# Performance work log

Measured on AMD Instinct MI355X. Metric: run time of the kernel, lower is better.

Reference implementation:

```python
import jax, jax.numpy as jnp
import numpy as np

BS, N_AGENTS, SA_DIM, HID = 2048, 64, 128, 256


def setup_inputs() -> dict:
    key = jax.random.key(0)
    ks = jax.random.split(key, 16)
    s = lambda fan_in: 1.0 / np.sqrt(fan_in)
    u = lambda k, shp, b: jax.random.uniform(k, shp, jnp.float32, -b, b)
    return {
        "x": jax.random.normal(ks[0], (BS, N_AGENTS, SA_DIM), jnp.float32),
        # encoder: Linear(sa, hid) -> Linear(hid, hid)
        "enc_w1": u(ks[1], (SA_DIM, HID), s(SA_DIM)),
        "enc_b1": u(ks[2], (HID,), s(SA_DIM)),
        "enc_w2": u(ks[3], (HID, HID), s(HID)),
        "enc_b2": u(ks[4], (HID,), s(HID)),
        # attention 'general' linear_in (no bias)
        "attn_w": u(ks[5], (HID, HID), s(HID)),
        # gc1: Linear(sa, hid); nn_gc1: Linear(sa, hid)
        "gc1_w": u(ks[6], (SA_DIM, HID), s(SA_DIM)),
        "gc1_b": u(ks[7], (HID,), s(SA_DIM)),
        "nn1_w": u(ks[8], (SA_DIM, HID), s(SA_DIM)),
        "nn1_b": u(ks[9], (HID,), s(SA_DIM)),
        # gc2: Linear(hid, hid); nn_gc2: Linear(hid, hid)
        "gc2_w": u(ks[10], (HID, HID), s(HID)),
        "gc2_b": u(ks[11], (HID,), s(HID)),
        "nn2_w": u(ks[12], (HID, HID), s(HID)),
        "nn2_b": u(ks[13], (HID,), s(HID)),
        "n_agents": N_AGENTS,
    }


def reference(x, enc_w1, enc_b1, enc_w2, enc_b2, attn_w,
              gc1_w, gc1_b, nn1_w, nn1_b, gc2_w, gc2_b, nn2_w, nn2_b,
              n_agents):
    relu = jax.nn.relu
    inv_n = 1.0 / n_agents
    # encoder MLP: relu(relu(x W1 + b1) W2 + b2)  -> [bs, n, hid]
    emb = relu(relu(x @ enc_w1 + enc_b1) @ enc_w2 + enc_b2)
    # general attention: softmax((emb W_a) emb^T) over last axis -> [bs, n, n]
    scores = jnp.einsum('bnd,bmd->bnm', emb @ attn_w, emb)
    attn = jax.nn.softmax(scores, axis=-1)
    # gc1: adj @ Linear(x); residual relu branch; normalize by n_agents
    feat = relu(jnp.einsum('bnm,bmh->bnh', attn, x @ gc1_w + gc1_b))
    feat = (feat + relu(x @ nn1_w + nn1_b)) * inv_n
    # gc2 on feat
    out = relu(jnp.einsum('bnm,bmh->bnh', attn, feat @ gc2_w + gc2_b))
    out = (out + relu(feat @ nn2_w + nn2_b)) * inv_n
    return out, attn
```

## Files before the change

kernel.cpp:

```cpp
#include <hip/hip_runtime.h>

typedef _Float16 half8 __attribute__((ext_vector_type(8)));
typedef _Float16 half4_t __attribute__((ext_vector_type(4)));
typedef float f32x4 __attribute__((ext_vector_type(4)));

#define NBATCH 2048
#define NA 64
#define SA 128
#define HID 256

#define OFF_X 0
#define OFF_R0 8192
#define OFF_ATT (8192 + 16384)
#define SMEM_BYTES ((8192 + 16384 + 8192) * 2)

#define W_ENC1 0
#define W_ENC2 (W_ENC1 + 128 * 256)
#define W_ATTN (W_ENC2 + 256 * 256)
#define W_GC1 (W_ATTN + 256 * 256)
#define W_NN1 (W_GC1 + 128 * 256)
#define W_GC2 (W_NN1 + 128 * 256)
#define W_NN2 (W_GC2 + 256 * 256)

#define MFMA(a, b, cacc) __builtin_amdgcn_mfma_f32_16x16x32_f16((a), (b), (cacc), 0, 0, 0)

__global__ void pack_all(const float* __restrict__ e1, const float* __restrict__ e2,
                         const float* __restrict__ aw, const float* __restrict__ g1,
                         const float* __restrict__ n1, const float* __restrict__ g2,
                         const float* __restrict__ n2, _Float16* __restrict__ dst) {
  int b = (int)blockIdx.x;
  const float* src;
  int off;
  if (b < 16) { src = e1; off = W_ENC1; }
  else if (b < 48) { src = e2; off = W_ENC2; b -= 16; }
  else if (b < 80) { src = aw; off = W_ATTN; b -= 48; }
  else if (b < 96) { src = g1; off = W_GC1; b -= 80; }
  else if (b < 112) { src = n1; off = W_NN1; b -= 96; }
  else if (b < 144) { src = g2; off = W_GC2; b -= 112; }
  else { src = n2; off = W_NN2; b -= 144; }
  int t = b * 256 + (int)threadIdx.x;
  int lane = t & 63, frag = t >> 6;
  int nt = frag & 15, kt = frag >> 4;
  int g = lane >> 4, c = lane & 15;
  half8 h;
#pragma unroll
  for (int j = 0; j < 8; ++j)
    h[j] = (_Float16)src[(size_t)(kt * 32 + g * 8 + j) * 256 + nt * 16 + c];
  *(half8*)(dst + off + (size_t)t * 8) = h;
}

__global__ __launch_bounds__(256, 2) void dicg_main(
    const float* __restrict__ x, const float* __restrict__ b_enc1,
    const float* __restrict__ b_enc2, const float* __restrict__ b_gc1,
    const float* __restrict__ b_nn1, const float* __restrict__ b_gc2,
    const float* __restrict__ b_nn2, const _Float16* __restrict__ wp,
    float* __restrict__ out, float* __restrict__ attn_out) {
  extern __shared__ _Float16 sm[];
  _Float16* X = sm + OFF_X;
  _Float16* R0 = sm + OFF_R0;
  _Float16* ATTp = sm + OFF_ATT;

  const int tid = (int)threadIdx.x;
  const int wv = tid >> 6;
  const int lane = tid & 63;
  const int g = lane >> 4;
  const int c = lane & 15;
  const int bb = (int)blockIdx.x;
  const float* __restrict__ xb = x + (size_t)bb * (NA * SA);

  auto ldA = [&](const _Float16* p, int kt, int rt) -> half8 {
    return *(const half8*)(p + (kt * 4 + rt) * 512 + lane * 8);
  };
  auto ldB = [&](const _Float16* p, int kt, int ct) -> half8 {
    return *(const half8*)(p + (kt * 16 + ct) * 512 + lane * 8);
  };
  auto wfrag = [&](const _Float16* wb, int kt, int ntg) -> half8 {
    return *(const half8*)(wb + ((size_t)(kt * 16 + ntg) * 64 + lane) * 8);
  };
  auto xfrag = [&](int r0, int k0) -> half8 {
    const float* p = xb + (r0 + c) * SA + k0 + g * 8;
    f32x4 u = *(const f32x4*)p;
    f32x4 v = *(const f32x4*)(p + 4);
    half8 h;
    h[0] = (_Float16)u[0]; h[1] = (_Float16)u[1];
    h[2] = (_Float16)u[2]; h[3] = (_Float16)u[3];
    h[4] = (_Float16)v[0]; h[5] = (_Float16)v[1];
    h[6] = (_Float16)v[2]; h[7] = (_Float16)v[3];
    return h;
  };

  auto stA_val = [&](_Float16* dst, int rt, int nt, int r, float v) {
    int kt = 2 * wv + (nt >> 1);
    int lanep = (2 * (nt & 1) + (c >> 3)) * 16 + 4 * g + r;
    dst[(kt * 4 + rt) * 512 + lanep * 8 + (c & 7)] = (_Float16)v;
  };
  auto ep_storeA = [&](f32x4(&acc)[4][4], const float* bias, bool dorelu) {
#pragma unroll
    for (int nt = 0; nt < 4; ++nt) {
      float bv = bias[64 * wv + 16 * nt + c];
#pragma unroll
      for (int rt = 0; rt < 4; ++rt)
#pragma unroll
        for (int r = 0; r < 4; ++r) {
          float y = acc[rt][nt][r] + bv;
          if (dorelu) y = fmaxf(y, 0.f);
          stA_val(R0, rt, nt, r, y);
        }
    }
  };
  auto ep_storeB = [&](f32x4(&acc)[4][4], const float* bias) {
#pragma unroll
    for (int nt = 0; nt < 4; ++nt) {
      float bv = bias[64 * wv + 16 * nt + c];
#pragma unroll
      for (int rt = 0; rt < 4; ++rt) {
        half4_t h;
#pragma unroll
        for (int r = 0; r < 4; ++r) h[r] = (_Float16)(acc[rt][nt][r] + bv);
        int fi = (rt >> 1) * 16 + 4 * wv + nt;
        int lanep = (2 * (rt & 1) + (g >> 1)) * 16 + c;
        *(half4_t*)(R0 + fi * 512 + lanep * 8 + 4 * (g & 1)) = h;
      }
    }
  };
  auto stQ = [&](const f32x4(&q2)[2], int s) {
    _Float16* base = ATTp + (8 + 2 * wv + s) * 512;
#pragma unroll
    for (int nt2 = 0; nt2 < 2; ++nt2)
#pragma unroll
      for (int r = 0; r < 4; ++r)
        base[((2 * nt2 + (c >> 3)) * 16 + 4 * g + r) * 8 + (c & 7)] = (_Float16)q2[nt2][r];
  };

  auto mmA = [&](f32x4(&acc)[4][4], const _Float16* Ap, const _Float16* wb, int nkt) {
#pragma unroll
    for (int kt = 0; kt < nkt; ++kt) {
      half8 af[4], bf[4];
#pragma unroll
      for (int rt = 0; rt < 4; ++rt) af[rt] = ldA(Ap, kt, rt);
#pragma unroll
      for (int nt = 0; nt < 4; ++nt) bf[nt] = wfrag(wb, kt, 4 * wv + nt);
#pragma unroll
      for (int rt = 0; rt < 4; ++rt)
#pragma unroll
        for (int nt = 0; nt < 4; ++nt) acc[rt][nt] = MFMA(af[rt], bf[nt], acc[rt][nt]);
    }
  };
  auto mmA2 = [&](f32x4(&a1)[4][4], f32x4(&a2)[4][4], const _Float16* Ap,
                  const _Float16* wb1, const _Float16* wb2, int nkt) {
#pragma unroll
    for (int kt = 0; kt < nkt; ++kt) {
      half8 af[4], b1[4], b2[4];
#pragma unroll
      for (int rt = 0; rt < 4; ++rt) af[rt] = ldA(Ap, kt, rt);
#pragma unroll
      for (int nt = 0; nt < 4; ++nt) b1[nt] = wfrag(wb1, kt, 4 * wv + nt);
#pragma unroll
      for (int nt = 0; nt < 4; ++nt) b2[nt] = wfrag(wb2, kt, 4 * wv + nt);
#pragma unroll
      for (int rt = 0; rt < 4; ++rt)
#pragma unroll
        for (int nt = 0; nt < 4; ++nt) {
          a1[rt][nt] = MFMA(af[rt], b1[nt], a1[rt][nt]);
          a2[rt][nt] = MFMA(af[rt], b2[nt], a2[rt][nt]);
        }
    }
  };
  auto mm_att = [&](f32x4(&acc)[4][4]) {
#pragma unroll
    for (int kt = 0; kt < 2; ++kt) {
      half8 af[4], bf[4];
#pragma unroll
      for (int rt = 0; rt < 4; ++rt) af[rt] = ldA(ATTp, kt, rt);
#pragma unroll
      for (int nt = 0; nt < 4; ++nt) bf[nt] = ldB(R0, kt, 4 * wv + nt);
#pragma unroll
      for (int rt = 0; rt < 4; ++rt)
#pragma unroll
        for (int nt = 0; nt < 4; ++nt) acc[rt][nt] = MFMA(af[rt], bf[nt], acc[rt][nt]);
    }
  };

  {
    f32x4 acc[4][4]{};
#pragma unroll
    for (int kt = 0; kt < 4; ++kt) {
      half8 af[4], bf[4];
#pragma unroll
      for (int rt = 0; rt < 4; ++rt) af[rt] = xfrag(16 * rt, kt * 32);
#pragma unroll
      for (int nt = 0; nt < 4; ++nt) bf[nt] = wfrag(wp + W_ENC1, kt, 4 * wv + nt);
      if (kt == wv) {
#pragma unroll
        for (int rt = 0; rt < 4; ++rt)
          *(half8*)(X + (kt * 4 + rt) * 512 + lane * 8) = af[rt];
      }
#pragma unroll
      for (int rt = 0; rt < 4; ++rt)
#pragma unroll
        for (int nt = 0; nt < 4; ++nt) acc[rt][nt] = MFMA(af[rt], bf[nt], acc[rt][nt]);
    }
    ep_storeA(acc, b_enc1, true);
  }
  __syncthreads();
  {
    f32x4 acc[4][4]{};
    mmA(acc, R0, wp + W_ENC2, 8);
    __syncthreads();
    ep_storeA(acc, b_enc2, true);
  }
  __syncthreads();
  {
    half8 aeK[8];
#pragma unroll
    for (int k2 = 0; k2 < 8; ++k2) aeK[k2] = ldA(R0, k2, wv);
    f32x4 sc[4]{};
    {
      f32x4 q2[2]{};
#pragma unroll
      for (int k2 = 0; k2 < 8; ++k2) {
        q2[0] = MFMA(aeK[k2], wfrag(wp + W_ATTN, k2, 0), q2[0]);
        q2[1] = MFMA(aeK[k2], wfrag(wp + W_ATTN, k2, 1), q2[1]);
      }
      stQ(q2, 0);
    }
#pragma unroll
    for (int ktp = 0; ktp < 8; ++ktp) {
      f32x4 q2n[2]{};
      if (ktp < 7) {
#pragma unroll
        for (int k2 = 0; k2 < 8; ++k2) {
          q2n[0] = MFMA(aeK[k2], wfrag(wp + W_ATTN, k2, 2 * ktp + 2), q2n[0]);
          q2n[1] = MFMA(aeK[k2], wfrag(wp + W_ATTN, k2, 2 * ktp + 3), q2n[1]);
        }
      }
      asm volatile("s_waitcnt lgkmcnt(0)" ::: "memory");
      half8 qb = *(const half8*)(ATTp + (8 + 2 * wv + (ktp & 1)) * 512 + lane * 8);
      if (ktp < 7) stQ(q2n, (ktp + 1) & 1);
#pragma unroll
      for (int rt = 0; rt < 4; ++rt) sc[rt] = MFMA(ldA(R0, ktp, rt), qb, sc[rt]);
    }
    float m = sc[0][0];
#pragma unroll
    for (int rt = 0; rt < 4; ++rt)
#pragma unroll
      for (int r = 0; r < 4; ++r) m = fmaxf(m, sc[rt][r]);
    m = fmaxf(m, __shfl_xor(m, 16));
    m = fmaxf(m, __shfl_xor(m, 32));
    float e[4][4], s = 0.f;
#pragma unroll
    for (int rt = 0; rt < 4; ++rt)
#pragma unroll
      for (int r = 0; r < 4; ++r) {
        e[rt][r] = __expf(sc[rt][r] - m);
        s += e[rt][r];
      }
    s += __shfl_xor(s, 16);
    s += __shfl_xor(s, 32);
    float inv = 1.0f / s;
    float* ao = attn_out + ((size_t)bb * NA + 16 * wv + c) * NA;
#pragma unroll
    for (int rt = 0; rt < 4; ++rt) {
      f32x4 vv;
      half4_t hh;
#pragma unroll
      for (int r = 0; r < 4; ++r) {
        vv[r] = e[rt][r] * inv;
        hh[r] = (_Float16)vv[r];
      }
      *(f32x4*)(ao + 16 * rt + 4 * g) = vv;
      int fi = (rt >> 1) * 4 + wv;
      int lanep = (2 * (rt & 1) + (g >> 1)) * 16 + c;
      *(half4_t*)(ATTp + fi * 512 + lanep * 8 + 4 * (g & 1)) = hh;
    }
  }
  __syncthreads();
  {
    f32x4 aG[4][4]{}, aN[4][4]{};
    mmA2(aG, aN, X, wp + W_GC1, wp + W_NN1, 4);
    ep_storeB(aG, b_gc1);
    half4_t r2h[4][4];
#pragma unroll
    for (int nt = 0; nt < 4; ++nt) {
      float bv = b_nn1[64 * wv + 16 * nt + c];
#pragma unroll
      for (int rt = 0; rt < 4; ++rt)
#pragma unroll
        for (int r = 0; r < 4; ++r)
          r2h[rt][nt][r] = (_Float16)fmaxf(aN[rt][nt][r] + bv, 0.f);
    }
    __syncthreads();
    f32x4 a1[4][4]{};
    mm_att(a1);
    __syncthreads();
#pragma unroll
    for (int nt = 0; nt < 4; ++nt)
#pragma unroll
      for (int rt = 0; rt < 4; ++rt)
#pragma unroll
        for (int r = 0; r < 4; ++r)
          stA_val(R0, rt, nt, r,
                  (fmaxf(a1[rt][nt][r], 0.f) + (float)r2h[rt][nt][r]) * 0.015625f);
  }
  __syncthreads();
  {
    f32x4 aN[4][4]{}, aG[4][4]{};
    mmA2(aN, aG, R0, wp + W_NN2, wp + W_GC2, 8);
    half4_t r2h[4][4];
#pragma unroll
    for (int nt = 0; nt < 4; ++nt) {
      float bv = b_nn2[64 * wv + 16 * nt + c];
#pragma unroll
      for (int rt = 0; rt < 4; ++rt)
#pragma unroll
        for (int r = 0; r < 4; ++r)
          r2h[rt][nt][r] = (_Float16)fmaxf(aN[rt][nt][r] + bv, 0.f);
    }
    __syncthreads();
    ep_storeB(aG, b_gc2);
    __syncthreads();
    f32x4 a1[4][4]{};
    mm_att(a1);
    float* ob = out + (size_t)bb * NA * HID;
#pragma unroll
    for (int nt = 0; nt < 4; ++nt)
#pragma unroll
      for (int rt = 0; rt < 4; ++rt)
#pragma unroll
        for (int r = 0; r < 4; ++r)
          ob[(size_t)(16 * rt + 4 * g + r) * HID + 64 * wv + 16 * nt + c] =
              (fmaxf(a1[rt][nt][r], 0.f) + (float)r2h[rt][nt][r]) * 0.015625f;
  }
}

extern "C" void kernel_launch(void* const* d_in, const int* in_sizes, int n_in,
                              void* d_out, int out_size, void* d_ws, size_t ws_size,
                              hipStream_t stream) {
  const float* x = (const float*)d_in[0];
  const float* enc_w1 = (const float*)d_in[1];
  const float* enc_b1 = (const float*)d_in[2];
  const float* enc_w2 = (const float*)d_in[3];
  const float* enc_b2 = (const float*)d_in[4];
  const float* attn_w = (const float*)d_in[5];
  const float* gc1_w = (const float*)d_in[6];
  const float* gc1_b = (const float*)d_in[7];
  const float* nn1_w = (const float*)d_in[8];
  const float* nn1_b = (const float*)d_in[9];
  const float* gc2_w = (const float*)d_in[10];
  const float* gc2_b = (const float*)d_in[11];
  const float* nn2_w = (const float*)d_in[12];
  const float* nn2_b = (const float*)d_in[13];

  _Float16* wp = (_Float16*)d_ws;
  float* out = (float*)d_out;
  float* attn_o = out + (size_t)NBATCH * NA * HID;

  pack_all<<<176, 256, 0, stream>>>(enc_w1, enc_w2, attn_w, gc1_w, nn1_w, gc2_w,
                                    nn2_w, wp);
  dicg_main<<<NBATCH, 256, SMEM_BYTES, stream>>>(
      x, enc_b1, enc_b2, gc1_b, nn1_b, gc2_b, nn2_b, wp, out, attn_o);
}
```

Measured before the change: 167.5 us.

## Compute transposed GEMM tiles so epilogues write packed half4 vectors

Swaps the MFMA operand order (weights as A, activations as B) so each lane holds four consecutive feature outputs. Epilogues can then convert and store half4 vectors to shared memory, load biases as float4, and write the final output as float4 rows instead of scalar half and float stores. It also splits the fused GC/NN matmuls into mixed-orientation passes and renames the fragment loads. This aims to cut LDS store instruction count and uncoalesced global writes, at the cost of more complex index mapping that must stay consistent across stages.

Measured after the change: 190.9 us. +13.9%, slower.

```diff
diff --git a/kernel.cpp b/kernel.cpp
--- a/kernel.cpp
+++ b/kernel.cpp
@@ -10,9 +10,9 @@
 #define HID 256
 
 #define OFF_X 0
-#define OFF_R0 8192
-#define OFF_ATT (8192 + 16384)
-#define SMEM_BYTES ((8192 + 16384 + 8192) * 2)
+#define OFF_R 8192
+#define OFF_ATT 24576
+#define SMEM_BYTES 65536
 
 #define W_ENC1 0
 #define W_ENC2 (W_ENC1 + 128 * 256)
@@ -57,8 +57,8 @@
     float* __restrict__ out, float* __restrict__ attn_out) {
   extern __shared__ _Float16 sm[];
   _Float16* X = sm + OFF_X;
-  _Float16* R0 = sm + OFF_R0;
-  _Float16* ATTp = sm + OFF_ATT;
+  _Float16* R = sm + OFF_R;
+  _Float16* AT = sm + OFF_ATT;
 
   const int tid = (int)threadIdx.x;
   const int wv = tid >> 6;
@@ -68,11 +68,8 @@
   const int bb = (int)blockIdx.x;
   const float* __restrict__ xb = x + (size_t)bb * (NA * SA);
 
-  auto ldA = [&](const _Float16* p, int kt, int rt) -> half8 {
-    return *(const half8*)(p + (kt * 4 + rt) * 512 + lane * 8);
-  };
-  auto ldB = [&](const _Float16* p, int kt, int ct) -> half8 {
-    return *(const half8*)(p + (kt * 16 + ct) * 512 + lane * 8);
+  auto ldF = [&](const _Float16* p, int fi) -> half8 {
+    return *(const half8*)(p + fi * 512 + lane * 8);
   };
   auto wfrag = [&](const _Float16* wb, int kt, int ntg) -> half8 {
     return *(const half8*)(wb + ((size_t)(kt * 16 + ntg) * 64 + lane) * 8);
@@ -89,247 +86,289 @@
     return h;
   };
 
-  auto stA_val = [&](_Float16* dst, int rt, int nt, int r, float v) {
-    int kt = 2 * wv + (nt >> 1);
-    int lanep = (2 * (nt & 1) + (c >> 3)) * 16 + 4 * g + r;
-    dst[(kt * 4 + rt) * 512 + lanep * 8 + (c & 7)] = (_Float16)v;
-  };
-  auto ep_storeA = [&](f32x4(&acc)[4][4], const float* bias, bool dorelu) {
+  auto stFS = [&](_Float16* p, int mt, int nt, half4_t hv) {
+    int fi = (2 * wv + (mt >> 1)) * 4 + nt;
+    int gt = (2 * mt + (g >> 1)) & 3;
+    *(half4_t*)(p + fi * 512 + (16 * gt + c) * 8 + 4 * (g & 1)) = hv;
+  };
+  auto stTS = [&](_Float16* p, int rt, int nt, half4_t hv) {
+    int fi = (rt >> 1) * 16 + 4 * wv + nt;
+    int gt = (2 * rt + (g >> 1)) & 3;
+    *(half4_t*)(p + fi * 512 + (16 * gt + c) * 8 + 4 * (g & 1)) = hv;
+  };
+  auto stQ = [&](const f32x4(&qa)[2], int slot) {
+    _Float16* base = AT + (8 + 2 * wv + slot) * 512;
+#pragma unroll
+    for (int t = 0; t < 2; ++t) {
+      half4_t hv;
+#pragma unroll
+      for (int r = 0; r < 4; ++r) hv[r] = (_Float16)qa[t][r];
+      int gt = (2 * t + (g >> 1)) & 3;
+      *(half4_t*)(base + (16 * gt + c) * 8 + 4 * (g & 1)) = hv;
+    }
+  };
+
+  {
+    f32x4 acc[4][4]{};
+#pragma unroll
+    for (int kt = 0; kt < 4; ++kt) {
+      half8 xf[4];
+#pragma unroll
+      for (int nt = 0; nt < 4; ++nt) xf[nt] = xfrag(16 * nt, kt * 32);
+      if (kt == wv) {
+#pragma unroll
+        for (int nt = 0; nt < 4; ++nt)
+          *(half8*)(X + (kt * 4 + nt) * 512 + lane * 8) = xf[nt];
+      }
+#pragma unroll
+      for (int mt = 0; mt < 4; ++mt) {
+        half8 wf = wfrag(wp + W_ENC1, kt, 4 * wv + mt);
+#pragma unroll
+        for (int nt = 0; nt < 4; ++nt) acc[mt][nt] = MFMA(wf, xf[nt], acc[mt][nt]);
+      }
+    }
+#pragma unroll
+    for (int mt = 0; mt < 4; ++mt) {
+      f32x4 bv = *(const f32x4*)(b_enc1 + 64 * wv + 16 * mt + 4 * g);
+#pragma unroll
+      for (int nt = 0; nt < 4; ++nt) {
+        half4_t hv;
+#pragma unroll
+        for (int r = 0; r < 4; ++r) hv[r] = (_Float16)fmaxf(acc[mt][nt][r] + bv[r], 0.f);
+        stFS(R, mt, nt, hv);
+      }
+    }
+  }
+  __syncthreads();
+  {
+    f32x4 acc[4][4]{};
+#pragma unroll
+    for (int kt = 0; kt < 8; ++kt) {
+      half8 bf[4];
+#pragma unroll
+      for (int nt = 0; nt < 4; ++nt) bf[nt] = ldF(R, kt * 4 + nt);
+#pragma unroll
+      for (int mt = 0; mt < 4; ++mt) {
+        half8 wf = wfrag(wp + W_ENC2, kt, 4 * wv + mt);
+#pragma unroll
+        for (int nt = 0; nt < 4; ++nt) acc[mt][nt] = MFMA(wf, bf[nt], acc[mt][nt]);
+      }
+    }
+    __syncthreads();
+#pragma unroll
+    for (int mt = 0; mt < 4; ++mt) {
+      f32x4 bv = *(const f32x4*)(b_enc2 + 64 * wv + 16 * mt + 4 * g);
+#pragma unroll
+      for (int nt = 0; nt < 4; ++nt) {
+        half4_t hv;
+#pragma unroll
+        for (int r = 0; r < 4; ++r) hv[r] = (_Float16)fmaxf(acc[mt][nt][r] + bv[r], 0.f);
+        stFS(R, mt, nt, hv);
+      }
+    }
+  }
+  __syncthreads();
+  {
+    half8 ebK[8];
+#pragma unroll
+    for (int kt = 0; kt < 8; ++kt) ebK[kt] = ldF(R, kt * 4 + wv);
+    f32x4 sc[4]{};
+    auto qtile = [&](int s, f32x4(&qa)[2]) {
+#pragma unroll
+      for (int kt = 0; kt < 8; ++kt) {
+        qa[0] = MFMA(wfrag(wp + W_ATTN, kt, 2 * s), ebK[kt], qa[0]);
+        qa[1] = MFMA(wfrag(wp + W_ATTN, kt, 2 * s + 1), ebK[kt], qa[1]);
+      }
+    };
+    {
+      f32x4 qa[2]{};
+      qtile(0, qa);
+      stQ(qa, 0);
+    }
+#pragma unroll
+    for (int s = 0; s < 8; ++s) {
+      f32x4 qn[2]{};
+      if (s < 7) qtile(s + 1, qn);
+      asm volatile("s_waitcnt lgkmcnt(0)" ::: "memory");
+      half8 qb = *(const half8*)(AT + (8 + 2 * wv + (s & 1)) * 512 + lane * 8);
+      if (s < 7) stQ(qn, (s + 1) & 1);
+#pragma unroll
+      for (int mt = 0; mt < 4; ++mt) sc[mt] = MFMA(ldF(R, s * 4 + mt), qb, sc[mt]);
+    }
+    float m0 = sc[0][0];
+#pragma unroll
+    for (int mt = 0; mt < 4; ++mt)
+#pragma unroll
+      for (int r = 0; r < 4; ++r) m0 = fmaxf(m0, sc[mt][r]);
+    m0 = fmaxf(m0, __shfl_xor(m0, 16));
+    m0 = fmaxf(m0, __shfl_xor(m0, 32));
+    float e[4][4], ssum = 0.f;
+#pragma unroll
+    for (int mt = 0; mt < 4; ++mt)
+#pragma unroll
+      for (int r = 0; r < 4; ++r) {
+        e[mt][r] = __expf(sc[mt][r] - m0);
+        ssum += e[mt][r];
+      }
+    ssum += __shfl_xor(ssum, 16);
+    ssum += __shfl_xor(ssum, 32);
+    float inv = 1.0f / ssum;
+    float* ao = attn_out + ((size_t)bb * NA + 16 * wv + c) * NA;
+#pragma unroll
+    for (int mt = 0; mt < 4; ++mt) {
+      f32x4 vv;
+      half4_t hv;
+#pragma unroll
+      for (int r = 0; r < 4; ++r) {
+        vv[r] = e[mt][r] * inv;
+        hv[r] = (_Float16)vv[r];
+      }
+      *(f32x4*)(ao + 16 * mt + 4 * g) = vv;
+      int fi = (mt >> 1) * 4 + wv;
+      int gt = (2 * mt + (g >> 1)) & 3;
+      *(half4_t*)(AT + fi * 512 + (16 * gt + c) * 8 + 4 * (g & 1)) = hv;
+    }
+  }
+  __syncthreads();
+  half4_t r1h[4][4];
+  {
+    f32x4 aG[4][4]{}, aN[4][4]{};
+#pragma unroll
+    for (int kt = 0; kt < 4; ++kt) {
+      half8 xf[4];
+#pragma unroll
+      for (int i = 0; i < 4; ++i) xf[i] = ldF(X, kt * 4 + i);
+#pragma unroll
+      for (int nt = 0; nt < 4; ++nt) {
+        half8 g1f = wfrag(wp + W_GC1, kt, 4 * wv + nt);
+#pragma unroll
+        for (int rt = 0; rt < 4; ++rt) aG[rt][nt] = MFMA(xf[rt], g1f, aG[rt][nt]);
+      }
+#pragma unroll
+      for (int mt = 0; mt < 4; ++mt) {
+        half8 n1f = wfrag(wp + W_NN1, kt, 4 * wv + mt);
+#pragma unroll
+        for (int nt = 0; nt < 4; ++nt) aN[mt][nt] = MFMA(n1f, xf[nt], aN[mt][nt]);
+      }
+    }
 #pragma unroll
     for (int nt = 0; nt < 4; ++nt) {
-      float bv = bias[64 * wv + 16 * nt + c];
-#pragma unroll
-      for (int rt = 0; rt < 4; ++rt)
-#pragma unroll
-        for (int r = 0; r < 4; ++r) {
-          float y = acc[rt][nt][r] + bv;
-          if (dorelu) y = fmaxf(y, 0.f);
-          stA_val(R0, rt, nt, r, y);
-        }
-    }
-  };
-  auto ep_storeB = [&](f32x4(&acc)[4][4], const float* bias) {
+      float bv = b_gc1[64 * wv + 16 * nt + c];
+#pragma unroll
+      for (int rt = 0; rt < 4; ++rt) {
+        half4_t hv;
+#pragma unroll
+        for (int r = 0; r < 4; ++r) hv[r] = (_Float16)(aG[rt][nt][r] + bv);
+        stTS(R, rt, nt, hv);
+      }
+    }
+#pragma unroll
+    for (int mt = 0; mt < 4; ++mt) {
+      f32x4 bv = *(const f32x4*)(b_nn1 + 64 * wv + 16 * mt + 4 * g);
+#pragma unroll
+      for (int nt = 0; nt < 4; ++nt)
+#pragma unroll
+        for (int r = 0; r < 4; ++r)
+          r1h[mt][nt][r] = (_Float16)fmaxf(aN[mt][nt][r] + bv[r], 0.f);
+    }
+  }
+  __syncthreads();
+  {
+    f32x4 a1[4][4]{};
+#pragma unroll
+    for (int kt = 0; kt < 2; ++kt) {
+      half8 atf[4];
+#pragma unroll
+      for (int nt = 0; nt < 4; ++nt) atf[nt] = ldF(AT, kt * 4 + nt);
+#pragma unroll
+      for (int mt = 0; mt < 4; ++mt) {
+        half8 xgf = ldF(R, kt * 16 + 4 * wv + mt);
+#pragma unroll
+        for (int nt = 0; nt < 4; ++nt) a1[mt][nt] = MFMA(xgf, atf[nt], a1[mt][nt]);
+      }
+    }
+    __syncthreads();
+#pragma unroll
+    for (int mt = 0; mt < 4; ++mt)
+#pragma unroll
+      for (int nt = 0; nt < 4; ++nt) {
+        half4_t hv;
+#pragma unroll
+        for (int r = 0; r < 4; ++r)
+          hv[r] = (_Float16)((fmaxf(a1[mt][nt][r], 0.f) + (float)r1h[mt][nt][r]) * 0.015625f);
+        stFS(R, mt, nt, hv);
+      }
+  }
+  __syncthreads();
+  half4_t r2h[4][4];
+  {
+    f32x4 aN2[4][4]{}, aG2[4][4]{};
+#pragma unroll
+    for (int kt = 0; kt < 8; ++kt) {
+      half8 ff[4];
+#pragma unroll
+      for (int i = 0; i < 4; ++i) ff[i] = ldF(R, kt * 4 + i);
+#pragma unroll
+      for (int mt = 0; mt < 4; ++mt) {
+        half8 n2f = wfrag(wp + W_NN2, kt, 4 * wv + mt);
+#pragma unroll
+        for (int nt = 0; nt < 4; ++nt) aN2[mt][nt] = MFMA(n2f, ff[nt], aN2[mt][nt]);
+      }
+#pragma unroll
+      for (int nt = 0; nt < 4; ++nt) {
+        half8 g2f = wfrag(wp + W_GC2, kt, 4 * wv + nt);
+#pragma unroll
+        for (int rt = 0; rt < 4; ++rt) aG2[rt][nt] = MFMA(ff[rt], g2f, aG2[rt][nt]);
+      }
+    }
+#pragma unroll
+    for (int mt = 0; mt < 4; ++mt) {
+      f32x4 bv = *(const f32x4*)(b_nn2 + 64 * wv + 16 * mt + 4 * g);
+#pragma unroll
+      for (int nt = 0; nt < 4; ++nt)
+#pragma unroll
+        for (int r = 0; r < 4; ++r)
+          r2h[mt][nt][r] = (_Float16)fmaxf(aN2[mt][nt][r] + bv[r], 0.f);
+    }
+    __syncthreads();
 #pragma unroll
     for (int nt = 0; nt < 4; ++nt) {
-      float bv = bias[64 * wv + 16 * nt + c];
+      float bv = b_gc2[64 * wv + 16 * nt + c];
 #pragma unroll
       for (int rt = 0; rt < 4; ++rt) {
-        half4_t h;
-#pragma unroll
-        for (int r = 0; r < 4; ++r) h[r] = (_Float16)(acc[rt][nt][r] + bv);
-        int fi = (rt >> 1) * 16 + 4 * wv + nt;
-        int lanep = (2 * (rt & 1) + (g >> 1)) * 16 + c;
-        *(half4_t*)(R0 + fi * 512 + lanep * 8 + 4 * (g & 1)) = h;
-      }
-    }
-  };
-  auto stQ = [&](const f32x4(&q2)[2], int s) {
-    _Float16* base = ATTp + (8 + 2 * wv + s) * 512;
-#pragma unroll
-    for (int nt2 = 0; nt2 < 2; ++nt2)
-#pragma unroll
-      for (int r = 0; r < 4; ++r)
-        base[((2 * nt2 + (c >> 3)) * 16 + 4 * g + r) * 8 + (c & 7)] = (_Float16)q2[nt2][r];
-  };
-
-  auto mmA = [&](f32x4(&acc)[4][4], const _Float16* Ap, const _Float16* wb, int nkt) {
-#pragma unroll
-    for (int kt = 0; kt < nkt; ++kt) {
-      half8 af[4], bf[4];
-#pragma unroll
-      for (int rt = 0; rt < 4; ++rt) af[rt] = ldA(Ap, kt, rt);
-#pragma unroll
-      for (int nt = 0; nt < 4; ++nt) bf[nt] = wfrag(wb, kt, 4 * wv + nt);
-#pragma unroll
-      for (int rt = 0; rt < 4; ++rt)
-#pragma unroll
-        for (int nt = 0; nt < 4; ++nt) acc[rt][nt] = MFMA(af[rt], bf[nt], acc[rt][nt]);
-    }
-  };
-  auto mmA2 = [&](f32x4(&a1)[4][4], f32x4(&a2)[4][4], const _Float16* Ap,
-                  const _Float16* wb1, const _Float16* wb2, int nkt) {
-#pragma unroll
-    for (int kt = 0; kt < nkt; ++kt) {
-      half8 af[4], b1[4], b2[4];
-#pragma unroll
-      for (int rt = 0; rt < 4; ++rt) af[rt] = ldA(Ap, kt, rt);
-#pragma unroll
-      for (int nt = 0; nt < 4; ++nt) b1[nt] = wfrag(wb1, kt, 4 * wv + nt);
-#pragma unroll
-      for (int nt = 0; nt < 4; ++nt) b2[nt] = wfrag(wb2, kt, 4 * wv + nt);
-#pragma unroll
-      for (int rt = 0; rt < 4; ++rt)
-#pragma unroll
-        for (int nt = 0; nt < 4; ++nt) {
-          a1[rt][nt] = MFMA(af[rt], b1[nt], a1[rt][nt]);
-          a2[rt][nt] = MFMA(af[rt], b2[nt], a2[rt][nt]);
-        }
-    }
-  };
-  auto mm_att = [&](f32x4(&acc)[4][4]) {
+        half4_t hv;
+#pragma unroll
+        for (int r = 0; r < 4; ++r) hv[r] = (_Float16)(aG2[rt][nt][r] + bv);
+        stTS(R, rt, nt, hv);
+      }
+    }
+  }
+  __syncthreads();
+  {
+    f32x4 a1[4][4]{};
 #pragma unroll
     for (int kt = 0; kt < 2; ++kt) {
-      half8 af[4], bf[4];
-#pragma unroll
-      for (int rt = 0; rt < 4; ++rt) af[rt] = ldA(ATTp, kt, rt);
-#pragma unroll
-      for (int nt = 0; nt < 4; ++nt) bf[nt] = ldB(R0, kt, 4 * wv + nt);
-#pragma unroll
-      for (int rt = 0; rt < 4; ++rt)
-#pragma unroll
-        for (int nt = 0; nt < 4; ++nt) acc[rt][nt] = MFMA(af[rt], bf[nt], acc[rt][nt]);
-    }
-  };
-
-  {
-    f32x4 acc[4][4]{};
-#pragma unroll
-    for (int kt = 0; kt < 4; ++kt) {
-      half8 af[4], bf[4];
-#pragma unroll
-      for (int rt = 0; rt < 4; ++rt) af[rt] = xfrag(16 * rt, kt * 32);
-#pragma unroll
-      for (int nt = 0; nt < 4; ++nt) bf[nt] = wfrag(wp + W_ENC1, kt, 4 * wv + nt);
-      if (kt == wv) {
-#pragma unroll
-        for (int rt = 0; rt < 4; ++rt)
-          *(half8*)(X + (kt * 4 + rt) * 512 + lane * 8) = af[rt];
-      }
-#pragma unroll
-      for (int rt = 0; rt < 4; ++rt)
-#pragma unroll
-        for (int nt = 0; nt < 4; ++nt) acc[rt][nt] = MFMA(af[rt], bf[nt], acc[rt][nt]);
-    }
-    ep_storeA(acc, b_enc1, true);
-  }
-  __syncthreads();
-  {
-    f32x4 acc[4][4]{};
-    mmA(acc, R0, wp + W_ENC2, 8);
-    __syncthreads();
-    ep_storeA(acc, b_enc2, true);
-  }
-  __syncthreads();
-  {
-    half8 aeK[8];
-#pragma unroll
-    for (int k2 = 0; k2 < 8; ++k2) aeK[k2] = ldA(R0, k2, wv);
-    f32x4 sc[4]{};
-    {
-      f32x4 q2[2]{};
-#pragma unroll
-      for (int k2 = 0; k2 < 8; ++k2) {
-        q2[0] = MFMA(aeK[k2], wfrag(wp + W_ATTN, k2, 0), q2[0]);
-        q2[1] = MFMA(aeK[k2], wfrag(wp + W_ATTN, k2, 1), q2[1]);
-      }
-      stQ(q2, 0);
-    }
-#pragma unroll
-    for (int ktp = 0; ktp < 8; ++ktp) {
-      f32x4 q2n[2]{};
-      if (ktp < 7) {
-#pragma unroll
-        for (int k2 = 0; k2 < 8; ++k2) {
-          q2n[0] = MFMA(aeK[k2], wfrag(wp + W_ATTN, k2, 2 * ktp + 2), q2n[0]);
-          q2n[1] = MFMA(aeK[k2], wfrag(wp + W_ATTN, k2, 2 * ktp + 3), q2n[1]);
-        }
-      }
-      asm volatile("s_waitcnt lgkmcnt(0)" ::: "memory");
-      half8 qb = *(const half8*)(ATTp + (8 + 2 * wv + (ktp & 1)) * 512 + lane * 8);
-      if (ktp < 7) stQ(q2n, (ktp + 1) & 1);
-#pragma unroll
-      for (int rt = 0; rt < 4; ++rt) sc[rt] = MFMA(ldA(R0, ktp, rt), qb, sc[rt]);
-    }
-    float m = sc[0][0];
-#pragma unroll
-    for (int rt = 0; rt < 4; ++rt)
-#pragma unroll
-      for (int r = 0; r < 4; ++r) m = fmaxf(m, sc[rt][r]);
-    m = fmaxf(m, __shfl_xor(m, 16));
-    m = fmaxf(m, __shfl_xor(m, 32));
-    float e[4][4], s = 0.f;
-#pragma unroll
-    for (int rt = 0; rt < 4; ++rt)
-#pragma unroll
-      for (int r = 0; r < 4; ++r) {
-        e[rt][r] = __expf(sc[rt][r] - m);
-        s += e[rt][r];
-      }
-    s += __shfl_xor(s, 16);
-    s += __shfl_xor(s, 32);
-    float inv = 1.0f / s;
-    float* ao = attn_out + ((size_t)bb * NA + 16 * wv + c) * NA;
-#pragma unroll
-    for (int rt = 0; rt < 4; ++rt) {
-      f32x4 vv;
-      half4_t hh;
-#pragma unroll
-      for (int r = 0; r < 4; ++r) {
-        vv[r] = e[rt][r] * inv;
-        hh[r] = (_Float16)vv[r];
-      }
-      *(f32x4*)(ao + 16 * rt + 4 * g) = vv;
-      int fi = (rt >> 1) * 4 + wv;
-      int lanep = (2 * (rt & 1) + (g >> 1)) * 16 + c;
-      *(half4_t*)(ATTp + fi * 512 + lanep * 8 + 4 * (g & 1)) = hh;
-    }
-  }
-  __syncthreads();
-  {
-    f32x4 aG[4][4]{}, aN[4][4]{};
-    mmA2(aG, aN, X, wp + W_GC1, wp + W_NN1, 4);
-    ep_storeB(aG, b_gc1);
-    half4_t r2h[4][4];
-#pragma unroll
-    for (int nt = 0; nt < 4; ++nt) {
-      float bv = b_nn1[64 * wv + 16 * nt + c];
-#pragma unroll
-      for (int rt = 0; rt < 4; ++rt)
+      half8 atf[4];
+#pragma unroll
+      for (int nt = 0; nt < 4; ++nt) atf[nt] = ldF(AT, kt * 4 + nt);
+#pragma unroll
+      for (int mt = 0; mt < 4; ++mt) {
+        half8 fgf = ldF(R, kt * 16 + 4 * wv + mt);
+#pragma unroll
+        for (int nt = 0; nt < 4; ++nt) a1[mt][nt] = MFMA(fgf, atf[nt], a1[mt][nt]);
+      }
+    }
+    float* ob = out + (size_t)bb * NA * HID;
+#pragma unroll
+    for (int mt = 0; mt < 4; ++mt)
+#pragma unroll
+      for (int nt = 0; nt < 4; ++nt) {
+        f32x4 vv;
 #pragma unroll
         for (int r = 0; r < 4; ++r)
-          r2h[rt][nt][r] = (_Float16)fmaxf(aN[rt][nt][r] + bv, 0.f);
-    }
-    __syncthreads();
-    f32x4 a1[4][4]{};
-    mm_att(a1);
-    __syncthreads();
-#pragma unroll
-    for (int nt = 0; nt < 4; ++nt)
-#pragma unroll
-      for (int rt = 0; rt < 4; ++rt)
-#pragma unroll
-        for (int r = 0; r < 4; ++r)
-          stA_val(R0, rt, nt, r,
-                  (fmaxf(a1[rt][nt][r], 0.f) + (float)r2h[rt][nt][r]) * 0.015625f);
-  }
-  __syncthreads();
-  {
-    f32x4 aN[4][4]{}, aG[4][4]{};
-    mmA2(aN, aG, R0, wp + W_NN2, wp + W_GC2, 8);
-    half4_t r2h[4][4];
-#pragma unroll
-    for (int nt = 0; nt < 4; ++nt) {
-      float bv = b_nn2[64 * wv + 16 * nt + c];
-#pragma unroll
-      for (int rt = 0; rt < 4; ++rt)
-#pragma unroll
-        for (int r = 0; r < 4; ++r)
-          r2h[rt][nt][r] = (_Float16)fmaxf(aN[rt][nt][r] + bv, 0.f);
-    }
-    __syncthreads();
-    ep_storeB(aG, b_gc2);
-    __syncthreads();
-    f32x4 a1[4][4]{};
-    mm_att(a1);
-    float* ob = out + (size_t)bb * NA * HID;
-#pragma unroll
-    for (int nt = 0; nt < 4; ++nt)
-#pragma unroll
-      for (int rt = 0; rt < 4; ++rt)
-#pragma unroll
-        for (int r = 0; r < 4; ++r)
-          ob[(size_t)(16 * rt + 4 * g + r) * HID + 64 * wv + 16 * nt + c] =
-              (fmaxf(a1[rt][nt][r], 0.f) + (float)r2h[rt][nt][r]) * 0.015625f;
+          vv[r] = (fmaxf(a1[mt][nt][r], 0.f) + (float)r2h[mt][nt][r]) * 0.015625f;
+        *(f32x4*)(ob + (size_t)(16 * nt + c) * HID + 64 * wv + 16 * mt + 4 * g) = vv;
+      }
   }
 }
 
```

## Drop shared X buffer, reload x from global, split dual GEMMs for occupancy

Applied to the files above, without the earlier changes.

Removes the shared-memory copy of x and re-reads x fragments from global memory for the gc1 and nn1 projections, cutting LDS from 64KB to 40KB. The paired dual-accumulator GEMMs are split into sequential single GEMMs to lower register pressure, and launch bounds are raised to 3 blocks per CU. The Q staging buffer is moved into the attention region. In exchange, x is read from global three times and the weight-fragment loads are no longer shared across the two GEMMs.

Result: slower. 244.6 us (+46.0%).

```diff
diff --git a/kernel.cpp b/kernel.cpp
--- a/kernel.cpp
+++ b/kernel.cpp
@@ -9,10 +9,9 @@
 #define SA 128
 #define HID 256
 
-#define OFF_X 0
-#define OFF_R0 8192
-#define OFF_ATT (8192 + 16384)
-#define SMEM_BYTES ((8192 + 16384 + 8192) * 2)
+#define OFF_R0 0
+#define OFF_ATT 16384
+#define SMEM_BYTES 40960
 
 #define W_ENC1 0
 #define W_ENC2 (W_ENC1 + 128 * 256)
@@ -49,14 +48,13 @@
   *(half8*)(dst + off + (size_t)t * 8) = h;
 }
 
-__global__ __launch_bounds__(256, 2) void dicg_main(
+__global__ __launch_bounds__(256, 3) void dicg_main(
     const float* __restrict__ x, const float* __restrict__ b_enc1,
     const float* __restrict__ b_enc2, const float* __restrict__ b_gc1,
     const float* __restrict__ b_nn1, const float* __restrict__ b_gc2,
     const float* __restrict__ b_nn2, const _Float16* __restrict__ wp,
     float* __restrict__ out, float* __restrict__ attn_out) {
   extern __shared__ _Float16 sm[];
-  _Float16* X = sm + OFF_X;
   _Float16* R0 = sm + OFF_R0;
   _Float16* ATTp = sm + OFF_ATT;
 
@@ -124,7 +122,7 @@
     }
   };
   auto stQ = [&](const f32x4(&q2)[2], int s) {
-    _Float16* base = ATTp + (8 + 2 * wv + s) * 512;
+    _Float16* base = ATTp + (wv + 4 * s) * 512;
 #pragma unroll
     for (int nt2 = 0; nt2 < 2; ++nt2)
 #pragma unroll
@@ -146,24 +144,18 @@
         for (int nt = 0; nt < 4; ++nt) acc[rt][nt] = MFMA(af[rt], bf[nt], acc[rt][nt]);
     }
   };
-  auto mmA2 = [&](f32x4(&a1)[4][4], f32x4(&a2)[4][4], const _Float16* Ap,
-                  const _Float16* wb1, const _Float16* wb2, int nkt) {
-#pragma unroll
-    for (int kt = 0; kt < nkt; ++kt) {
-      half8 af[4], b1[4], b2[4];
-#pragma unroll
-      for (int rt = 0; rt < 4; ++rt) af[rt] = ldA(Ap, kt, rt);
-#pragma unroll
-      for (int nt = 0; nt < 4; ++nt) b1[nt] = wfrag(wb1, kt, 4 * wv + nt);
-#pragma unroll
-      for (int nt = 0; nt < 4; ++nt) b2[nt] = wfrag(wb2, kt, 4 * wv + nt);
-#pragma unroll
-      for (int rt = 0; rt < 4; ++rt)
-#pragma unroll
-        for (int nt = 0; nt < 4; ++nt) {
-          a1[rt][nt] = MFMA(af[rt], b1[nt], a1[rt][nt]);
-          a2[rt][nt] = MFMA(af[rt], b2[nt], a2[rt][nt]);
-        }
+  auto mm_x = [&](f32x4(&acc)[4][4], const _Float16* wb) {
+#pragma unroll
+    for (int kt = 0; kt < 4; ++kt) {
+      half8 af[4], bf[4];
+#pragma unroll
+      for (int rt = 0; rt < 4; ++rt) af[rt] = xfrag(16 * rt, kt * 32);
+#pragma unroll
+      for (int nt = 0; nt < 4; ++nt) bf[nt] = wfrag(wb, kt, 4 * wv + nt);
+#pragma unroll
+      for (int rt = 0; rt < 4; ++rt)
+#pragma unroll
+        for (int nt = 0; nt < 4; ++nt) acc[rt][nt] = MFMA(af[rt], bf[nt], acc[rt][nt]);
     }
   };
   auto mm_att = [&](f32x4(&acc)[4][4]) {
@@ -183,23 +175,7 @@
 
   {
     f32x4 acc[4][4]{};
-#pragma unroll
-    for (int kt = 0; kt < 4; ++kt) {
-      half8 af[4], bf[4];
-#pragma unroll
-      for (int rt = 0; rt < 4; ++rt) af[rt] = xfrag(16 * rt, kt * 32);
-#pragma unroll
-      for (int nt = 0; nt < 4; ++nt) bf[nt] = wfrag(wp + W_ENC1, kt, 4 * wv + nt);
-      if (kt == wv) {
-#pragma unroll
-        for (int rt = 0; rt < 4; ++rt)
-          *(half8*)(X + (kt * 4 + rt) * 512 + lane * 8) = af[rt];
-      }
-#pragma unroll
-      for (int rt = 0; rt < 4; ++rt)
-#pragma unroll
-        for (int nt = 0; nt < 4; ++nt) acc[rt][nt] = MFMA(af[rt], bf[nt], acc[rt][nt]);
-    }
+    mm_x(acc, wp + W_ENC1);
     ep_storeA(acc, b_enc1, true);
   }
   __syncthreads();
@@ -235,7 +211,7 @@
         }
       }
       asm volatile("s_waitcnt lgkmcnt(0)" ::: "memory");
-      half8 qb = *(const half8*)(ATTp + (8 + 2 * wv + (ktp & 1)) * 512 + lane * 8);
+      half8 qb = *(const half8*)(ATTp + (wv + 4 * (ktp & 1)) * 512 + lane * 8);
       if (ktp < 7) stQ(q2n, (ktp + 1) & 1);
 #pragma unroll
       for (int rt = 0; rt < 4; ++rt) sc[rt] = MFMA(ldA(R0, ktp, rt), qb, sc[rt]);
@@ -275,11 +251,15 @@
     }
   }
   __syncthreads();
-  {
-    f32x4 aG[4][4]{}, aN[4][4]{};
-    mmA2(aG, aN, X, wp + W_GC1, wp + W_NN1, 4);
+  half4_t r1h[4][4];
+  {
+    f32x4 aG[4][4]{};
+    mm_x(aG, wp + W_GC1);
     ep_storeB(aG, b_gc1);
-    half4_t r2h[4][4];
+  }
+  {
+    f32x4 aN[4][4]{};
+    mm_x(aN, wp + W_NN1);
 #pragma unroll
     for (int nt = 0; nt < 4; ++nt) {
       float bv = b_nn1[64 * wv + 16 * nt + c];
@@ -287,9 +267,11 @@
       for (int rt = 0; rt < 4; ++rt)
 #pragma unroll
         for (int r = 0; r < 4; ++r)
-          r2h[rt][nt][r] = (_Float16)fmaxf(aN[rt][nt][r] + bv, 0.f);
-    }
-    __syncthreads();
+          r1h[rt][nt][r] = (_Float16)fmaxf(aN[rt][nt][r] + bv, 0.f);
+    }
+  }
+  __syncthreads();
+  {
     f32x4 a1[4][4]{};
     mm_att(a1);
     __syncthreads();
@@ -300,13 +282,13 @@
 #pragma unroll
         for (int r = 0; r < 4; ++r)
           stA_val(R0, rt, nt, r,
-                  (fmaxf(a1[rt][nt][r], 0.f) + (float)r2h[rt][nt][r]) * 0.015625f);
-  }
-  __syncthreads();
-  {
-    f32x4 aN[4][4]{}, aG[4][4]{};
-    mmA2(aN, aG, R0, wp + W_NN2, wp + W_GC2, 8);
-    half4_t r2h[4][4];
+                  (fmaxf(a1[rt][nt][r], 0.f) + (float)r1h[rt][nt][r]) * 0.015625f);
+  }
+  __syncthreads();
+  half4_t r2h[4][4];
+  {
+    f32x4 aN2[4][4]{};
+    mmA(aN2, R0, wp + W_NN2, 8);
 #pragma unroll
     for (int nt = 0; nt < 4; ++nt) {
       float bv = b_nn2[64 * wv + 16 * nt + c];
@@ -314,11 +296,17 @@
       for (int rt = 0; rt < 4; ++rt)
 #pragma unroll
         for (int r = 0; r < 4; ++r)
-          r2h[rt][nt][r] = (_Float16)fmaxf(aN[rt][nt][r] + bv, 0.f);
-    }
+          r2h[rt][nt][r] = (_Float16)fmaxf(aN2[rt][nt][r] + bv, 0.f);
+    }
+  }
+  {
+    f32x4 aG2[4][4]{};
+    mmA(aG2, R0, wp + W_GC2, 8);
     __syncthreads();
-    ep_storeB(aG, b_gc2);
-    __syncthreads();
+    ep_storeB(aG2, b_gc2);
+  }
+  __syncthreads();
+  {
     f32x4 a1[4][4]{};
     mm_att(a1);
     float* ob = out + (size_t)bb * NA * HID;
```

## Prefetch next-stage weight fragments across barriers and use LDS-only barriers

Applied to the files above, without the earlier changes.

Loads the first k-slices of each upcoming stage's weight fragments from global memory into registers before the preceding barrier or epilogue, so their latency overlaps earlier work. __syncthreads is replaced with a barrier that waits only on LDS counters (lgkmcnt), so outstanding global loads do not have to drain at each sync. This raises register pressure and may reduce occupancy or cause spills.

Measured after the change: 156.4 us. 6.6% less time.

```diff
diff --git a/kernel.cpp b/kernel.cpp
--- a/kernel.cpp
+++ b/kernel.cpp
@@ -23,6 +23,12 @@
 #define W_NN2 (W_GC2 + 256 * 256)
 
 #define MFMA(a, b, cacc) __builtin_amdgcn_mfma_f32_16x16x32_f16((a), (b), (cacc), 0, 0, 0)
+
+#define BAR()                                            \
+  do {                                                   \
+    asm volatile("s_waitcnt lgkmcnt(0)" ::: "memory");   \
+    __builtin_amdgcn_s_barrier();                        \
+  } while (0)
 
 __global__ void pack_all(const float* __restrict__ e1, const float* __restrict__ e2,
                          const float* __restrict__ aw, const float* __restrict__ g1,
@@ -131,41 +137,6 @@
       for (int r = 0; r < 4; ++r)
         base[((2 * nt2 + (c >> 3)) * 16 + 4 * g + r) * 8 + (c & 7)] = (_Float16)q2[nt2][r];
   };
-
-  auto mmA = [&](f32x4(&acc)[4][4], const _Float16* Ap, const _Float16* wb, int nkt) {
-#pragma unroll
-    for (int kt = 0; kt < nkt; ++kt) {
-      half8 af[4], bf[4];
-#pragma unroll
-      for (int rt = 0; rt < 4; ++rt) af[rt] = ldA(Ap, kt, rt);
-#pragma unroll
-      for (int nt = 0; nt < 4; ++nt) bf[nt] = wfrag(wb, kt, 4 * wv + nt);
-#pragma unroll
-      for (int rt = 0; rt < 4; ++rt)
-#pragma unroll
-        for (int nt = 0; nt < 4; ++nt) acc[rt][nt] = MFMA(af[rt], bf[nt], acc[rt][nt]);
-    }
-  };
-  auto mmA2 = [&](f32x4(&a1)[4][4], f32x4(&a2)[4][4], const _Float16* Ap,
-                  const _Float16* wb1, const _Float16* wb2, int nkt) {
-#pragma unroll
-    for (int kt = 0; kt < nkt; ++kt) {
-      half8 af[4], b1[4], b2[4];
-#pragma unroll
-      for (int rt = 0; rt < 4; ++rt) af[rt] = ldA(Ap, kt, rt);
-#pragma unroll
-      for (int nt = 0; nt < 4; ++nt) b1[nt] = wfrag(wb1, kt, 4 * wv + nt);
-#pragma unroll
-      for (int nt = 0; nt < 4; ++nt) b2[nt] = wfrag(wb2, kt, 4 * wv + nt);
-#pragma unroll
-      for (int rt = 0; rt < 4; ++rt)
-#pragma unroll
-        for (int nt = 0; nt < 4; ++nt) {
-          a1[rt][nt] = MFMA(af[rt], b1[nt], a1[rt][nt]);
-          a2[rt][nt] = MFMA(af[rt], b2[nt], a2[rt][nt]);
-        }
-    }
-  };
   auto mm_att = [&](f32x4(&acc)[4][4]) {
 #pragma unroll
     for (int kt = 0; kt < 2; ++kt) {
@@ -181,6 +152,11 @@
     }
   };
 
+  half8 pf2[2][4];
+  half8 pfq[4][2];
+  half8 pf5g[4], pf5n[4];
+  half8 pf7n[2][4], pf7g[2][4];
+
   {
     f32x4 acc[4][4]{};
 #pragma unroll
@@ -200,16 +176,37 @@
 #pragma unroll
         for (int nt = 0; nt < 4; ++nt) acc[rt][nt] = MFMA(af[rt], bf[nt], acc[rt][nt]);
     }
+#pragma unroll
+    for (int s = 0; s < 2; ++s)
+#pragma unroll
+      for (int nt = 0; nt < 4; ++nt) pf2[s][nt] = wfrag(wp + W_ENC2, s, 4 * wv + nt);
     ep_storeA(acc, b_enc1, true);
   }
-  __syncthreads();
+  BAR();
   {
     f32x4 acc[4][4]{};
-    mmA(acc, R0, wp + W_ENC2, 8);
-    __syncthreads();
+#pragma unroll
+    for (int kt = 0; kt < 8; ++kt) {
+      half8 af[4], bf[4];
+#pragma unroll
+      for (int rt = 0; rt < 4; ++rt) af[rt] = ldA(R0, kt, rt);
+#pragma unroll
+      for (int nt = 0; nt < 4; ++nt)
+        bf[nt] = (kt < 2) ? pf2[kt][nt] : wfrag(wp + W_ENC2, kt, 4 * wv + nt);
+#pragma unroll
+      for (int rt = 0; rt < 4; ++rt)
+#pragma unroll
+        for (int nt = 0; nt < 4; ++nt) acc[rt][nt] = MFMA(af[rt], bf[nt], acc[rt][nt]);
+    }
+#pragma unroll
+    for (int k2 = 0; k2 < 4; ++k2) {
+      pfq[k2][0] = wfrag(wp + W_ATTN, k2, 0);
+      pfq[k2][1] = wfrag(wp + W_ATTN, k2, 1);
+    }
+    BAR();
     ep_storeA(acc, b_enc2, true);
   }
-  __syncthreads();
+  BAR();
   {
     half8 aeK[8];
 #pragma unroll
@@ -219,8 +216,10 @@
       f32x4 q2[2]{};
 #pragma unroll
       for (int k2 = 0; k2 < 8; ++k2) {
-        q2[0] = MFMA(aeK[k2], wfrag(wp + W_ATTN, k2, 0), q2[0]);
-        q2[1] = MFMA(aeK[k2], wfrag(wp + W_ATTN, k2, 1), q2[1]);
+        half8 b0 = (k2 < 4) ? pfq[k2][0] : wfrag(wp + W_ATTN, k2, 0);
+        half8 b1 = (k2 < 4) ? pfq[k2][1] : wfrag(wp + W_ATTN, k2, 1);
+        q2[0] = MFMA(aeK[k2], b0, q2[0]);
+        q2[1] = MFMA(aeK[k2], b1, q2[1]);
       }
       stQ(q2, 0);
     }
@@ -258,6 +257,11 @@
     s += __shfl_xor(s, 16);
     s += __shfl_xor(s, 32);
     float inv = 1.0f / s;
+#pragma unroll
+    for (int nt = 0; nt < 4; ++nt) {
+      pf5g[nt] = wfrag(wp + W_GC1, 0, 4 * wv + nt);
+      pf5n[nt] = wfrag(wp + W_NN1, 0, 4 * wv + nt);
+    }
     float* ao = attn_out + ((size_t)bb * NA + 16 * wv + c) * NA;
 #pragma unroll
     for (int rt = 0; rt < 4; ++rt) {
@@ -274,12 +278,30 @@
       *(half4_t*)(ATTp + fi * 512 + lanep * 8 + 4 * (g & 1)) = hh;
     }
   }
-  __syncthreads();
+  BAR();
+  half4_t r1h[4][4];
   {
     f32x4 aG[4][4]{}, aN[4][4]{};
-    mmA2(aG, aN, X, wp + W_GC1, wp + W_NN1, 4);
+#pragma unroll
+    for (int kt = 0; kt < 4; ++kt) {
+      half8 af[4], b1[4], b2[4];
+#pragma unroll
+      for (int rt = 0; rt < 4; ++rt) af[rt] = ldA(X, kt, rt);
+#pragma unroll
+      for (int nt = 0; nt < 4; ++nt)
+        b1[nt] = (kt == 0) ? pf5g[nt] : wfrag(wp + W_GC1, kt, 4 * wv + nt);
+#pragma unroll
+      for (int nt = 0; nt < 4; ++nt)
+        b2[nt] = (kt == 0) ? pf5n[nt] : wfrag(wp + W_NN1, kt, 4 * wv + nt);
+#pragma unroll
+      for (int rt = 0; rt < 4; ++rt)
+#pragma unroll
+        for (int nt = 0; nt < 4; ++nt) {
+          aG[rt][nt] = MFMA(af[rt], b1[nt], aG[rt][nt]);
+          aN[rt][nt] = MFMA(af[rt], b2[nt], aN[rt][nt]);
+        }
+    }
     ep_storeB(aG, b_gc1);
-    half4_t r2h[4][4];
 #pragma unroll
     for (int nt = 0; nt < 4; ++nt) {
       float bv = b_nn1[64 * wv + 16 * nt + c];
@@ -287,12 +309,21 @@
       for (int rt = 0; rt < 4; ++rt)
 #pragma unroll
         for (int r = 0; r < 4; ++r)
-          r2h[rt][nt][r] = (_Float16)fmaxf(aN[rt][nt][r] + bv, 0.f);
-    }
-    __syncthreads();
+          r1h[rt][nt][r] = (_Float16)fmaxf(aN[rt][nt][r] + bv, 0.f);
+    }
+#pragma unroll
+    for (int s2 = 0; s2 < 2; ++s2)
+#pragma unroll
+      for (int nt = 0; nt < 4; ++nt) {
+        pf7n[s2][nt] = wfrag(wp + W_NN2, s2, 4 * wv + nt);
+        pf7g[s2][nt] = wfrag(wp + W_GC2, s2, 4 * wv + nt);
+      }
+  }
+  BAR();
+  {
     f32x4 a1[4][4]{};
     mm_att(a1);
-    __syncthreads();
+    BAR();
 #pragma unroll
     for (int nt = 0; nt < 4; ++nt)
 #pragma unroll
@@ -300,13 +331,31 @@
 #pragma unroll
         for (int r = 0; r < 4; ++r)
           stA_val(R0, rt, nt, r,
-                  (fmaxf(a1[rt][nt][r], 0.f) + (float)r2h[rt][nt][r]) * 0.015625f);
-  }
-  __syncthreads();
-  {
-    f32x4 aN[4][4]{}, aG[4][4]{};
-    mmA2(aN, aG, R0, wp + W_NN2, wp + W_GC2, 8);
-    half4_t r2h[4][4];
+                  (fmaxf(a1[rt][nt][r], 0.f) + (float)r1h[rt][nt][r]) * 0.015625f);
+  }
+  BAR();
+  half4_t r2h[4][4];
+  {
+    f32x4 aN2[4][4]{}, aG2[4][4]{};
+#pragma unroll
+    for (int kt = 0; kt < 8; ++kt) {
+      half8 af[4], b1[4], b2[4];
+#pragma unroll
+      for (int rt = 0; rt < 4; ++rt) af[rt] = ldA(R0, kt, rt);
+#pragma unroll
+      for (int nt = 0; nt < 4; ++nt)
+        b1[nt] = (kt < 2) ? pf7n[kt][nt] : wfrag(wp + W_NN2, kt, 4 * wv + nt);
+#pragma unroll
+      for (int nt = 0; nt < 4; ++nt)
+        b2[nt] = (kt < 2) ? pf7g[kt][nt] : wfrag(wp + W_GC2, kt, 4 * wv + nt);
+#pragma unroll
+      for (int rt = 0; rt < 4; ++rt)
+#pragma unroll
+        for (int nt = 0; nt < 4; ++nt) {
+          aN2[rt][nt] = MFMA(af[rt], b1[nt], aN2[rt][nt]);
+          aG2[rt][nt] = MFMA(af[rt], b2[nt], aG2[rt][nt]);
+        }
+    }
 #pragma unroll
     for (int nt = 0; nt < 4; ++nt) {
       float bv = b_nn2[64 * wv + 16 * nt + c];
@@ -314,11 +363,13 @@
       for (int rt = 0; rt < 4; ++rt)
 #pragma unroll
         for (int r = 0; r < 4; ++r)
-          r2h[rt][nt][r] = (_Float16)fmaxf(aN[rt][nt][r] + bv, 0.f);
-    }
-    __syncthreads();
-    ep_storeB(aG, b_gc2);
-    __syncthreads();
+          r2h[rt][nt][r] = (_Float16)fmaxf(aN2[rt][nt][r] + bv, 0.f);
+    }
+    BAR();
+    ep_storeB(aG2, b_gc2);
+  }
+  BAR();
+  {
     f32x4 a1[4][4]{};
     mm_att(a1);
     float* ob = out + (size_t)bb * NA * HID;
```
